# Performance work log

Hardware: AMD Instinct MI355X
Metric: run time of the kernel (lower is better)

The kernel has to match this reference:

```python
import jax, jax.numpy as jnp
import numpy as np

B, S, D, H, DH = 2, 1024, 1024, 16, 64
SCALE = 1.0 / np.sqrt(DH)


def setup_inputs() -> dict:
    key = jax.random.key(0)
    ks = jax.random.split(key, 9)
    return {
        "x": jax.random.normal(ks[0], (B, S, D), jnp.float32),
        "qkv_w": jax.random.normal(ks[1], (3 * H * DH, D), jnp.float32) * 0.02,
        "out_w": jax.random.normal(ks[2], (D, H * DH), jnp.float32) * 0.02,
        "bias_p": jax.random.uniform(ks[3], (H, 1, 1), jnp.float32) * 2.0,
        "bias_a": jax.random.uniform(ks[4], (H, 1, 1), jnp.float32),
        "mlp_w1": jax.random.normal(ks[5], (H, 2 * H), jnp.float32) * 0.1,
        "mlp_b1": jnp.zeros((H,), jnp.float32),
        "mlp_w2": jax.random.normal(ks[6], (H, H), jnp.float32) * 0.1,
        "mlp_b2": jnp.zeros((H,), jnp.float32),
    }


def reference(x, qkv_w, out_w, bias_p, bias_a, mlp_w1, mlp_b1, mlp_w2, mlp_b2):
    # qkv projection: torch Linear => x @ W.T
    qkv = (x @ qkv_w.T).reshape(B, S, 3, H, DH)
    q = qkv[:, :, 0].transpose(0, 2, 1, 3)  # [B,H,S,DH]
    k = qkv[:, :, 1].transpose(0, 2, 1, 3)
    v = qkv[:, :, 2].transpose(0, 2, 1, 3)

    scores = jnp.einsum('bhqd,bhkd->bhqk', q, k) * SCALE  # [B,H,S,S]

    # Kerple additive bias: -p * log1p(a * |i-j|), per head
    p = jnp.clip(bias_p, 0.01)
    a = jnp.clip(bias_a, 0.01)
    pos = jnp.arange(S, dtype=jnp.float32)
    dist = jnp.abs(pos[None, :] - pos[:, None])  # [S,S]
    kb = -p * jnp.log1p(a * dist)  # [H,S,S]

    # DAPE refinement MLP over per-(i,j) head features
    z = jnp.concatenate(
        [scores, jnp.broadcast_to(kb[None], (B, H, S, S))], axis=1
    ).transpose(0, 2, 3, 1)  # [B,S,S,2H]
    hdn = jax.nn.gelu(z @ mlp_w1.T + mlp_b1, approximate=False)  # [B,S,S,H]
    refine = (hdn @ mlp_w2.T + mlp_b2).transpose(0, 3, 1, 2)  # [B,H,S,S]

    scores = scores + kb[None] + refine
    attn = jax.nn.softmax(scores, axis=-1)  # dropout is identity in eval

    out = jnp.einsum('bhqk,bhkd->bhqd', attn, v)  # [B,H,S,DH]
    out = out.transpose(0, 2, 1, 3).reshape(B, S, H * DH)
    return out @ out_w.T
```

## Files before the change

kernel.cpp:

```cpp
#include <hip/hip_runtime.h>
#include <math.h>

#define Bsz 2
#define Ssz 1024
#define Dsz 1024
#define Hn 16
#define DHsz 64
#define QKV3 3072
#define SCALE 0.125f

typedef __bf16 bf16;
typedef bf16 bf16x8 __attribute__((ext_vector_type(8)));
typedef bf16 bf16x4 __attribute__((ext_vector_type(4)));
typedef float f32x4 __attribute__((ext_vector_type(4)));

#define MFMA(a, b, c) __builtin_amdgcn_mfma_f32_16x16x32_bf16(a, b, c, 0, 0, 0)
#define LDT 72

__global__ void cast_hilo(const float* __restrict__ src, bf16* __restrict__ hi,
                          bf16* __restrict__ lo, int n) {
  int idx = (blockIdx.x * 256 + threadIdx.x) * 4;
  if (idx >= n) return;
  float4 v = *(const float4*)(src + idx);
  bf16 h0 = (bf16)v.x, h1 = (bf16)v.y, h2 = (bf16)v.z, h3 = (bf16)v.w;
  bf16x4 hv = {h0, h1, h2, h3};
  bf16x4 lv = {(bf16)(v.x - (float)h0), (bf16)(v.y - (float)h1),
               (bf16)(v.z - (float)h2), (bf16)(v.w - (float)h3)};
  *(bf16x4*)(hi + idx) = hv;
  *(bf16x4*)(lo + idx) = lv;
}

__global__ void cast_hi(const float* __restrict__ src, bf16* __restrict__ hi, int n) {
  int idx = (blockIdx.x * 256 + threadIdx.x) * 4;
  if (idx >= n) return;
  float4 v = *(const float4*)(src + idx);
  bf16x4 hv = {(bf16)v.x, (bf16)v.y, (bf16)v.z, (bf16)v.w};
  *(bf16x4*)(hi + idx) = hv;
}

__global__ void kb_table(const float* __restrict__ bias_p, const float* __restrict__ bias_a,
                         float* __restrict__ kbtt) {
  int idx = blockIdx.x * 256 + threadIdx.x;
  int d = idx >> 4, h = idx & 15;
  float p = fmaxf(bias_p[h], 0.01f), a = fmaxf(bias_a[h], 0.01f);
  kbtt[idx] = -p * log1pf(a * (float)d);
}

__global__ void tk_table(const float* __restrict__ kbtt, const float* __restrict__ w1,
                         const float* __restrict__ b1, float2* __restrict__ tk) {
  int idx = blockIdx.x * 256 + threadIdx.x;
  int o = idx >> 4, n = idx & 15;
  int d = o - 1024; if (d < 0) d = -d; if (d > 1023) d = 1023;
  float t1 = b1[n];
#pragma unroll
  for (int h = 0; h < 16; ++h) t1 += w1[n * 32 + 16 + h] * kbtt[d * 16 + h];
  tk[idx] = make_float2(t1, kbtt[d * 16 + n]);
}

__global__ void wfrag(const float* __restrict__ w1, const float* __restrict__ w2,
                      bf16* __restrict__ wf) {
  int lane = threadIdx.x;
  int l15 = lane & 15, q8 = (lane >> 4) << 3;
  bf16x8 w1d, w2a;
#pragma unroll
  for (int e = 0; e < 8; ++e) {
    int k = q8 + e;
    if (k < 16) {
      w1d[e] = (bf16)w1[l15 * 32 + k];
    } else {
      float w = w1[l15 * 32 + k - 16];
      w1d[e] = (bf16)(w - (float)(bf16)w);
    }
    w2a[e] = (bf16)w2[l15 * 16 + (k & 15)];
  }
  *(bf16x8*)(wf + lane * 8) = w1d;
  *(bf16x8*)(wf + 512 + lane * 8) = w2a;
}

__global__ __launch_bounds__(256, 2) void k1_qkv(const bf16* __restrict__ A,
                                                 const bf16* __restrict__ Bh,
                                                 const bf16* __restrict__ Bl,
                                                 bf16* __restrict__ C) {
  __shared__ __align__(16) bf16 sA[128 * LDT];
  __shared__ __align__(16) bf16 sBh[96 * LDT], sBl[96 * LDT];
  const int tid = threadIdx.x;
  const int lane = tid & 63, wv = tid >> 6;
  const int wr = wv >> 1, wc = wv & 1;
  const int l15 = lane & 15, q8 = (lane >> 4) << 3, q4 = (lane >> 4) << 2;
  const int m0 = blockIdx.y * 128, n0 = blockIdx.x * 96;
  const int r0 = tid >> 3, c8 = (tid & 7) << 3;

  f32x4 acc[4][3];
#pragma unroll
  for (int t = 0; t < 4; ++t)
#pragma unroll
    for (int u = 0; u < 3; ++u)
#pragma unroll
      for (int r = 0; r < 4; ++r) acc[t][u][r] = 0.f;

  bf16x8 rA[4], rBh[3], rBl[3];
#define K1_LOAD(kt)                                                         \
  {                                                                         \
    _Pragma("unroll") for (int c = 0; c < 4; ++c)                           \
      rA[c] = *(const bf16x8*)(A + (size_t)(m0 + c * 32 + r0) * Dsz + (kt) + c8);  \
    _Pragma("unroll") for (int c = 0; c < 3; ++c) {                         \
      rBh[c] = *(const bf16x8*)(Bh + (size_t)(n0 + c * 32 + r0) * Dsz + (kt) + c8); \
      rBl[c] = *(const bf16x8*)(Bl + (size_t)(n0 + c * 32 + r0) * Dsz + (kt) + c8); \
    }                                                                       \
  }

  K1_LOAD(0)
  for (int kt = 0; kt < Dsz; kt += 64) {
    __syncthreads();
#pragma unroll
    for (int c = 0; c < 4; ++c) *(bf16x8*)&sA[(c * 32 + r0) * LDT + c8] = rA[c];
#pragma unroll
    for (int c = 0; c < 3; ++c) {
      *(bf16x8*)&sBh[(c * 32 + r0) * LDT + c8] = rBh[c];
      *(bf16x8*)&sBl[(c * 32 + r0) * LDT + c8] = rBl[c];
    }
    __syncthreads();
    if (kt + 64 < Dsz) K1_LOAD(kt + 64)
#pragma unroll
    for (int ks = 0; ks < 64; ks += 32) {
      bf16x8 fa[4], fbh[3], fbl[3];
#pragma unroll
      for (int t = 0; t < 4; ++t)
        fa[t] = *(const bf16x8*)&sA[(wr * 64 + t * 16 + l15) * LDT + ks + q8];
#pragma unroll
      for (int u = 0; u < 3; ++u) {
        int n = wc * 48 + u * 16 + l15;
        fbh[u] = *(const bf16x8*)&sBh[n * LDT + ks + q8];
        fbl[u] = *(const bf16x8*)&sBl[n * LDT + ks + q8];
      }
#pragma unroll
      for (int t = 0; t < 4; ++t)
#pragma unroll
        for (int u = 0; u < 3; ++u) {
          acc[t][u] = MFMA(fa[t], fbh[u], acc[t][u]);
          acc[t][u] = MFMA(fa[t], fbl[u], acc[t][u]);
        }
    }
  }
#pragma unroll
  for (int t = 0; t < 4; ++t)
#pragma unroll
    for (int u = 0; u < 3; ++u) {
      int col = n0 + wc * 48 + u * 16 + l15;
#pragma unroll
      for (int r = 0; r < 4; ++r) {
        int row = m0 + wr * 64 + t * 16 + q4 + r;
        C[(size_t)row * QKV3 + col] = (bf16)acc[t][u][r];
      }
    }
#undef K1_LOAD
}

__global__ void pack_vt(const bf16* __restrict__ qkv, bf16* __restrict__ vt) {
  __shared__ __align__(16) bf16 T[64 * LDT];
  const int tid = threadIdx.x;
  const int bh = blockIdx.y, b = bh >> 4, h = bh & 15;
  const int j0 = blockIdx.x * 64;
#pragma unroll
  for (int c = 0; c < 2; ++c) {
    int lin = c * 256 + tid;
    int jr = lin >> 3, d8 = (lin & 7) << 3;
    bf16x8 v = *(const bf16x8*)(qkv + (size_t)(b * Ssz + j0 + jr) * QKV3 + 2048 + h * DHsz + d8);
#pragma unroll
    for (int e = 0; e < 8; ++e) T[(d8 + e) * LDT + jr] = v[e];
  }
  __syncthreads();
#pragma unroll
  for (int c = 0; c < 2; ++c) {
    int lin = c * 256 + tid;
    int d = lin >> 3, j8 = (lin & 7) << 3;
    bf16x8 o = *(const bf16x8*)&T[d * LDT + j8];
    *(bf16x8*)(vt + ((size_t)(b * Hn + h) * DHsz + d) * Ssz + j0 + j8) = o;
  }
}

__global__ __launch_bounds__(256, 3) void k2_qk(const bf16* __restrict__ qkv,
                                                bf16* __restrict__ scores) {
  __shared__ __align__(16) bf16 sA[128 * LDT], sB[128 * LDT];
  const int tid = threadIdx.x;
  const int lane = tid & 63, wv = tid >> 6;
  const int wr = wv >> 1, wc = wv & 1;
  const int l15 = lane & 15, q8 = (lane >> 4) << 3, q4 = (lane >> 4) << 2;
  const int z = blockIdx.z, b = z >> 4, h = z & 15;
  const int i0 = blockIdx.y * 128, j0 = blockIdx.x * 128;
  const bf16* Ab = qkv + (size_t)b * Ssz * QKV3 + h * DHsz;
  const bf16* Bb = Ab + Ssz;
  const int r0 = tid >> 3, c8 = (tid & 7) << 3;
#pragma unroll
  for (int c = 0; c < 4; ++c) {
    int row = c * 32 + r0;
    *(bf16x8*)&sA[row * LDT + c8] = *(const bf16x8*)(Ab + (size_t)(i0 + row) * QKV3 + c8);
    *(bf16x8*)&sB[row * LDT + c8] = *(const bf16x8*)(Bb + (size_t)(j0 + row) * QKV3 + c8);
  }
  __syncthreads();
  f32x4 acc[4][4];
#pragma unroll
  for (int t = 0; t < 4; ++t)
#pragma unroll
    for (int u = 0; u < 4; ++u)
#pragma unroll
      for (int r = 0; r < 4; ++r) acc[t][u][r] = 0.f;
#pragma unroll
  for (int ks = 0; ks < 64; ks += 32) {
    bf16x8 fa[4], fb[4];
#pragma unroll
    for (int t = 0; t < 4; ++t) fa[t] = *(const bf16x8*)&sA[(wr * 64 + t * 16 + l15) * LDT + ks + q8];
#pragma unroll
    for (int u = 0; u < 4; ++u) fb[u] = *(const bf16x8*)&sB[(wc * 64 + u * 16 + l15) * LDT + ks + q8];
#pragma unroll
    for (int t = 0; t < 4; ++t)
#pragma unroll
      for (int u = 0; u < 4; ++u) acc[t][u] = MFMA(fa[t], fb[u], acc[t][u]);
  }
  bf16* dstp = scores + ((size_t)(b * Hn + h) << 20);
#pragma unroll
  for (int t = 0; t < 4; ++t)
#pragma unroll
    for (int u = 0; u < 4; ++u) {
      int col = j0 + wc * 64 + u * 16 + l15;
#pragma unroll
      for (int r = 0; r < 4; ++r) {
        int row = i0 + wr * 64 + t * 16 + q4 + r;
        dstp[((size_t)row << 10) + col] = (bf16)(acc[t][u][r] * SCALE);
      }
    }
}

__device__ __forceinline__ float gelu_fast(float x) {
  float z = fabsf(x) * 0.70710678118654752f;
  float t = __builtin_amdgcn_rcpf(fmaf(0.3275911f, z, 1.0f));
  float poly = t * fmaf(t, fmaf(t, fmaf(t, fmaf(t, 1.061405429f, -1.453152027f),
                                        1.421413741f), -0.284496736f), 0.254829592f);
  float erfa = 1.0f - poly * __expf(-z * z);
  float erfs = copysignf(erfa, x);
  return 0.5f * x * (1.0f + erfs);
}

#define SHS 264

__global__ __launch_bounds__(256, 8) void dape_softmax(bf16* scores,
                                                       const float2* __restrict__ tk,
                                                       const bf16* __restrict__ wf,
                                                       const float* __restrict__ b2,
                                                       float* __restrict__ sums) {
  const int c = blockIdx.x;
  const int i = blockIdx.y;
  const int b = blockIdx.z;
  const int tid = threadIdx.x;
  const int lane = tid & 63, wv = tid >> 6;
  const int l15 = lane & 15, q = lane >> 4;
  const int q8 = q << 3, q4 = q << 2;

  __shared__ bf16 sH[Hn][SHS];
  __shared__ __align__(16) bf16 hdnS[4][16][40];

  const bf16x8 w1d = *(const bf16x8*)(wf + lane * 8);
  const bf16x8 w2a = *(const bf16x8*)(wf + 512 + lane * 8);
  const float bias2 = b2[l15];

  if (lane < 32) {
    int row = lane >> 1, col = 16 + (lane & 1) * 8;
    *(bf16x8*)&hdnS[wv][row][col] = (bf16x8){};
  }

  const int jw = wv * 64;
  const bf16* srow = scores + ((size_t)(b * Hn) << 20) + ((size_t)i << 10) + c * 256;
#pragma unroll
  for (int t = 0; t < 2; ++t) {
    int h = t * 8 + (lane >> 3);
    int col = jw + (lane & 7) * 8;
    *(bf16x8*)&sH[h][col] = *(const bf16x8*)(srow + ((size_t)h << 20) + col);
  }

  const float2* tkp = tk + ((size_t)(c * 256 + jw + q4 - i + 1024) << 4) + l15;
  bf16* dsth = scores + ((size_t)(b * Hn + l15) << 20) + ((size_t)i << 10) + c * 256;
  float s_acc = 0.f;

  for (int jt = 0; jt < 4; ++jt) {
    const int j0c = jw + jt * 16;
    bf16x8 a1;
#pragma unroll
    for (int e = 0; e < 8; ++e) a1[e] = sH[(q8 + e) & 15][j0c + l15];
    float2 tkv[4];
#pragma unroll
    for (int r = 0; r < 4; ++r) tkv[r] = tkp[r * 16];
    f32x4 c1 = {tkv[0].x, tkv[1].x, tkv[2].x, tkv[3].x};
    c1 = MFMA(a1, w1d, c1);
#pragma unroll
    for (int r = 0; r < 4; ++r) hdnS[wv][q4 + r][l15] = (bf16)gelu_fast(c1[r]);
    bf16x8 a2 = *(const bf16x8*)&hdnS[wv][l15][q8];
    f32x4 c2 = {bias2, bias2, bias2, bias2};
    c2 = MFMA(a2, w2a, c2);
    bf16x4 sc4 = *(const bf16x4*)&sH[l15][j0c + q4];
    bf16x4 pv;
#pragma unroll
    for (int r = 0; r < 4; ++r) {
      float lg = (float)sc4[r] + tkv[r].y + c2[r];
      float e = __expf(lg);
      pv[r] = (bf16)e;
      s_acc += e;
    }
    *(bf16x4*)(dsth + j0c + q4) = pv;
    tkp += 256;
  }

  s_acc += __shfl_xor(s_acc, 16, 64);
  s_acc += __shfl_xor(s_acc, 32, 64);
  if (lane < 16) atomicAdd(&sums[(((b << 10) + i) << 4) + lane], s_acc);
}

__global__ __launch_bounds__(256, 4) void k4_av(const bf16* __restrict__ attn,
                                                const bf16* __restrict__ vt,
                                                const float* __restrict__ sums,
                                                bf16* __restrict__ aout) {
  __shared__ __align__(16) bf16 sA[64 * LDT], sB[64 * LDT];
  const int tid = threadIdx.x;
  const int lane = tid & 63, wv = tid >> 6;
  const int wr = wv >> 1, wc = wv & 1;
  const int l15 = lane & 15, q8 = (lane >> 4) << 3, q4 = (lane >> 4) << 2;
  const int i0 = blockIdx.x * 64, h = blockIdx.y, b = blockIdx.z;
  const bf16* Ab = attn + ((size_t)(b * Hn + h) << 20) + ((size_t)i0 << 10);
  const bf16* Bb = vt + (size_t)(b * Hn + h) * DHsz * Ssz;
  const int r0 = tid >> 3, c8 = (tid & 7) << 3;
  f32x4 acc[2][2];
#pragma unroll
  for (int t = 0; t < 2; ++t)
#pragma unroll
    for (int u = 0; u < 2; ++u)
#pragma unroll
      for (int r = 0; r < 4; ++r) acc[t][u][r] = 0.f;
  bf16x8 rA[2], rB[2];
#define K4_LOAD(kt)                                               \
  {                                                               \
    _Pragma("unroll") for (int c = 0; c < 2; ++c) {               \
      int row = c * 32 + r0;                                      \
      rA[c] = *(const bf16x8*)(Ab + ((size_t)row << 10) + (kt) + c8); \
      rB[c] = *(const bf16x8*)(Bb + ((size_t)row << 10) + (kt) + c8); \
    }                                                             \
  }
  K4_LOAD(0)
  for (int kt = 0; kt < Ssz; kt += 64) {
    __syncthreads();
#pragma unroll
    for (int c = 0; c < 2; ++c) {
      int row = c * 32 + r0;
      *(bf16x8*)&sA[row * LDT + c8] = rA[c];
      *(bf16x8*)&sB[row * LDT + c8] = rB[c];
    }
    __syncthreads();
    if (kt + 64 < Ssz) K4_LOAD(kt + 64)
#pragma unroll
    for (int ks = 0; ks < 64; ks += 32) {
      bf16x8 fa[2], fb[2];
#pragma unroll
      for (int t = 0; t < 2; ++t) fa[t] = *(const bf16x8*)&sA[(wr * 32 + t * 16 + l15) * LDT + ks + q8];
#pragma unroll
      for (int u = 0; u < 2; ++u) fb[u] = *(const bf16x8*)&sB[(wc * 32 + u * 16 + l15) * LDT + ks + q8];
#pragma unroll
      for (int t = 0; t < 2; ++t)
#pragma unroll
        for (int u = 0; u < 2; ++u) acc[t][u] = MFMA(fa[t], fb[u], acc[t][u]);
    }
  }
#pragma unroll
  for (int t = 0; t < 2; ++t)
#pragma unroll
    for (int r = 0; r < 4; ++r) {
      int row = i0 + wr * 32 + t * 16 + q4 + r;
      float inv = 1.f / sums[(((b << 10) + row) << 4) + h];
#pragma unroll
      for (int u = 0; u < 2; ++u) {
        int d = wc * 32 + u * 16 + l15;
        aout[(size_t)(b * Ssz + row) * Dsz + h * DHsz + d] = (bf16)(acc[t][u][r] * inv);
      }
    }
#undef K4_LOAD
}

__global__ __launch_bounds__(256, 3) void k5_out(const bf16* __restrict__ A,
                                                 const bf16* __restrict__ Bh,
                                                 const bf16* __restrict__ Bl,
                                                 float* __restrict__ C) {
  __shared__ __align__(16) bf16 sA[64 * LDT], sBh[64 * LDT], sBl[64 * LDT];
  const int tid = threadIdx.x;
  const int lane = tid & 63, wv = tid >> 6;
  const int wr = wv >> 1, wc = wv & 1;
  const int l15 = lane & 15, q8 = (lane >> 4) << 3, q4 = (lane >> 4) << 2;
  const int m0 = blockIdx.y * 64, n0 = blockIdx.x * 64;
  const int r0 = tid >> 3, c8 = (tid & 7) << 3;
  f32x4 acc[2][2];
#pragma unroll
  for (int t = 0; t < 2; ++t)
#pragma unroll
    for (int u = 0; u < 2; ++u)
#pragma unroll
      for (int r = 0; r < 4; ++r) acc[t][u][r] = 0.f;
  bf16x8 rA[2], rBh[2], rBl[2];
#define K5_LOAD(kt)                                                       \
  {                                                                       \
    _Pragma("unroll") for (int c = 0; c < 2; ++c) {                       \
      int row = c * 32 + r0;                                              \
      rA[c] = *(const bf16x8*)(A + (size_t)(m0 + row) * Dsz + (kt) + c8);   \
      rBh[c] = *(const bf16x8*)(Bh + (size_t)(n0 + row) * Dsz + (kt) + c8); \
      rBl[c] = *(const bf16x8*)(Bl + (size_t)(n0 + row) * Dsz + (kt) + c8); \
    }                                                                     \
  }
  K5_LOAD(0)
  for (int kt = 0; kt < Dsz; kt += 64) {
    __syncthreads();
#pragma unroll
    for (int c = 0; c < 2; ++c) {
      int row = c * 32 + r0;
      *(bf16x8*)&sA[row * LDT + c8] = rA[c];
      *(bf16x8*)&sBh[row * LDT + c8] = rBh[c];
      *(bf16x8*)&sBl[row * LDT + c8] = rBl[c];
    }
    __syncthreads();
    if (kt + 64 < Dsz) K5_LOAD(kt + 64)
#pragma unroll
    for (int ks = 0; ks < 64; ks += 32) {
      bf16x8 fa[2], fbh[2], fbl[2];
#pragma unroll
      for (int t = 0; t < 2; ++t) fa[t] = *(const bf16x8*)&sA[(wr * 32 + t * 16 + l15) * LDT + ks + q8];
#pragma unroll
      for (int u = 0; u < 2; ++u) {
        int n = wc * 32 + u * 16 + l15;
        fbh[u] = *(const bf16x8*)&sBh[n * LDT + ks + q8];
        fbl[u] = *(const bf16x8*)&sBl[n * LDT + ks + q8];
      }
#pragma unroll
      for (int t = 0; t < 2; ++t)
#pragma unroll
        for (int u = 0; u < 2; ++u) {
          acc[t][u] = MFMA(fa[t], fbh[u], acc[t][u]);
          acc[t][u] = MFMA(fa[t], fbl[u], acc[t][u]);
        }
    }
  }
#pragma unroll
  for (int t = 0; t < 2; ++t)
#pragma unroll
    for (int u = 0; u < 2; ++u) {
      int col = n0 + wc * 32 + u * 16 + l15;
#pragma unroll
      for (int r = 0; r < 4; ++r) {
        int row = m0 + wr * 32 + t * 16 + q4 + r;
        C[(size_t)row * Dsz + col] = acc[t][u][r];
      }
    }
#undef K5_LOAD
}

extern "C" void kernel_launch(void* const* d_in, const int* in_sizes, int n_in,
                              void* d_out, int out_size, void* d_ws, size_t ws_size,
                              hipStream_t stream) {
  const float* x      = (const float*)d_in[0];
  const float* qkv_w  = (const float*)d_in[1];
  const float* out_w  = (const float*)d_in[2];
  const float* bias_p = (const float*)d_in[3];
  const float* bias_a = (const float*)d_in[4];
  const float* w1     = (const float*)d_in[5];
  const float* b1     = (const float*)d_in[6];
  const float* w2     = (const float*)d_in[7];
  const float* b2     = (const float*)d_in[8];
  float* out = (float*)d_out;

  char* ws = (char*)d_ws;
  const size_t MB = 1ull << 20;
  bf16* ow_h   = (bf16*)(ws + 0 * MB);
  bf16* ow_l   = (bf16*)(ws + 2 * MB);
  bf16* qkv_bf = (bf16*)(ws + 4 * MB);
  bf16* v_t    = (bf16*)(ws + 16 * MB);
  bf16* aout   = (bf16*)(ws + 20 * MB);
  float* kbtt  = (float*)(ws + 24 * MB);
  float* sums  = (float*)(ws + 24 * MB + 65536);
  bf16* wf     = (bf16*)(ws + 24 * MB + 196608);
  float2* tk   = (float2*)(ws + 24 * MB + 262144);
  bf16* x_h    = (bf16*)(ws + 25 * MB);
  bf16* w_h    = (bf16*)(ws + 29 * MB);
  bf16* w_l    = (bf16*)(ws + 35 * MB);
  bf16* sc_bf  = (bf16*)(ws + 25 * MB);

  cast_hi<<<2048, 256, 0, stream>>>(x, x_h, Bsz * Ssz * Dsz);
  cast_hilo<<<3072, 256, 0, stream>>>(qkv_w, w_h, w_l, QKV3 * Dsz);
  cast_hilo<<<1024, 256, 0, stream>>>(out_w, ow_h, ow_l, Dsz * Dsz);
  kb_table<<<64, 256, 0, stream>>>(bias_p, bias_a, kbtt);
  tk_table<<<128, 256, 0, stream>>>(kbtt, w1, b1, tk);
  wfrag<<<1, 64, 0, stream>>>(w1, w2, wf);
  hipMemsetAsync(sums, 0, Bsz * Ssz * Hn * sizeof(float), stream);

  k1_qkv<<<dim3(QKV3 / 96, (Bsz * Ssz) / 128), 256, 0, stream>>>(x_h, w_h, w_l, qkv_bf);
  pack_vt<<<dim3(Ssz / 64, Bsz * Hn), 256, 0, stream>>>(qkv_bf, v_t);

  k2_qk<<<dim3(Ssz / 128, Ssz / 128, Bsz * Hn), 256, 0, stream>>>(qkv_bf, sc_bf);
  dape_softmax<<<dim3(4, Ssz, Bsz), 256, 0, stream>>>(sc_bf, tk, wf, b2, sums);
  k4_av<<<dim3(Ssz / 64, Hn, Bsz), 256, 0, stream>>>(sc_bf, v_t, sums, aout);

  k5_out<<<dim3(Dsz / 64, (Bsz * Ssz) / 64), 256, 0, stream>>>(aout, ow_h, ow_l, out);
}
```

Before: 234.8 us.

## Stage DAPE logits in LDS for coalesced per-head softmax stores

The DAPE softmax kernel now writes the per-head logits to a float LDS tile, synchronises, and then has each wave exponentiate and store full contiguous 256-element head rows. This replaces scattered 4-element bf16 stores spread across 16 heads. Per-chunk partial sums go to distinct slots instead of global atomics, so the memset of the sums buffer is dropped and k4_av adds the four partials itself. The extra LDS tile and the lower launch bound reduce occupancy and add a block barrier.

```diff
diff --git a/kernel.cpp b/kernel.cpp
--- a/kernel.cpp
+++ b/kernel.cpp
@@ -242,8 +242,9 @@
 }
 
 #define SHS 264
-
-__global__ __launch_bounds__(256, 8) void dape_softmax(bf16* scores,
+#define LGS 264
+
+__global__ __launch_bounds__(256, 5) void dape_softmax(bf16* scores,
                                                        const float2* __restrict__ tk,
                                                        const bf16* __restrict__ wf,
                                                        const float* __restrict__ b2,
@@ -257,6 +258,7 @@
   const int q8 = q << 3, q4 = q << 2;
 
   __shared__ bf16 sH[Hn][SHS];
+  __shared__ float lgt[Hn][LGS];
   __shared__ __align__(16) bf16 hdnS[4][16][40];
 
   const bf16x8 w1d = *(const bf16x8*)(wf + lane * 8);
@@ -278,8 +280,6 @@
   }
 
   const float2* tkp = tk + ((size_t)(c * 256 + jw + q4 - i + 1024) << 4) + l15;
-  bf16* dsth = scores + ((size_t)(b * Hn + l15) << 20) + ((size_t)i << 10) + c * 256;
-  float s_acc = 0.f;
 
   for (int jt = 0; jt < 4; ++jt) {
     const int j0c = jw + jt * 16;
@@ -297,21 +297,28 @@
     f32x4 c2 = {bias2, bias2, bias2, bias2};
     c2 = MFMA(a2, w2a, c2);
     bf16x4 sc4 = *(const bf16x4*)&sH[l15][j0c + q4];
-    bf16x4 pv;
-#pragma unroll
-    for (int r = 0; r < 4; ++r) {
-      float lg = (float)sc4[r] + tkv[r].y + c2[r];
-      float e = __expf(lg);
-      pv[r] = (bf16)e;
-      s_acc += e;
-    }
-    *(bf16x4*)(dsth + j0c + q4) = pv;
+    f32x4 lg;
+#pragma unroll
+    for (int r = 0; r < 4; ++r) lg[r] = (float)sc4[r] + tkv[r].y + c2[r];
+    *(f32x4*)&lgt[l15][j0c + q4] = lg;
     tkp += 256;
   }
-
-  s_acc += __shfl_xor(s_acc, 16, 64);
-  s_acc += __shfl_xor(s_acc, 32, 64);
-  if (lane < 16) atomicAdd(&sums[(((b << 10) + i) << 4) + lane], s_acc);
+  __syncthreads();
+
+#pragma unroll
+  for (int hh = 0; hh < 4; ++hh) {
+    const int h = wv * 4 + hh;
+    f32x4 v0 = *(const f32x4*)&lgt[h][lane * 4];
+    float s = 0.f;
+#pragma unroll
+    for (int e = 0; e < 4; ++e) { v0[e] = __expf(v0[e]); s += v0[e]; }
+#pragma unroll
+    for (int off = 32; off > 0; off >>= 1) s += __shfl_xor(s, off, 64);
+    bf16* dst = scores + ((size_t)(b * Hn + h) << 20) + ((size_t)i << 10) + c * 256;
+    bf16x4 p0 = {(bf16)v0[0], (bf16)v0[1], (bf16)v0[2], (bf16)v0[3]};
+    *(bf16x4*)(dst + lane * 4) = p0;
+    if (lane == 0) sums[((((b << 10) + i) << 4) + h) * 4 + c] = s;
+  }
 }
 
 __global__ __launch_bounds__(256, 4) void k4_av(const bf16* __restrict__ attn,
@@ -372,7 +379,8 @@
 #pragma unroll
     for (int r = 0; r < 4; ++r) {
       int row = i0 + wr * 32 + t * 16 + q4 + r;
-      float inv = 1.f / sums[(((b << 10) + row) << 4) + h];
+      f32x4 sv = *(const f32x4*)&sums[((((b << 10) + row) << 4) + h) * 4];
+      float inv = 1.f / (sv[0] + sv[1] + sv[2] + sv[3]);
 #pragma unroll
       for (int u = 0; u < 2; ++u) {
         int d = wc * 32 + u * 16 + l15;
@@ -479,8 +487,8 @@
   bf16* aout   = (bf16*)(ws + 20 * MB);
   float* kbtt  = (float*)(ws + 24 * MB);
   float* sums  = (float*)(ws + 24 * MB + 65536);
-  bf16* wf     = (bf16*)(ws + 24 * MB + 196608);
-  float2* tk   = (float2*)(ws + 24 * MB + 262144);
+  bf16* wf     = (bf16*)(ws + 24 * MB + 589824);
+  float2* tk   = (float2*)(ws + 24 * MB + 655360);
   bf16* x_h    = (bf16*)(ws + 25 * MB);
   bf16* w_h    = (bf16*)(ws + 29 * MB);
   bf16* w_l    = (bf16*)(ws + 35 * MB);
@@ -492,7 +500,6 @@
   kb_table<<<64, 256, 0, stream>>>(bias_p, bias_a, kbtt);
   tk_table<<<128, 256, 0, stream>>>(kbtt, w1, b1, tk);
   wfrag<<<1, 64, 0, stream>>>(w1, w2, wf);
-  hipMemsetAsync(sums, 0, Bsz * Ssz * Hn * sizeof(float), stream);
 
   k1_qkv<<<dim3(QKV3 / 96, (Bsz * Ssz) / 128), 256, 0, stream>>>(x_h, w_h, w_l, qkv_bf);
   pack_vt<<<dim3(Ssz / 64, Bsz * Hn), 256, 0, stream>>>(qkv_bf, v_t);
```

New measurement: 217.6 us. -7.3%, faster.
